# Performance work log

Hardware: AMD Instinct MI355X
Metric: run time of the kernel (lower is better)

## Reference

```python
import jax, jax.numpy as jnp
import numpy as np
import math

HIDDEN = 768
HEADS = 12
HEAD_DIM = HIDDEN // HEADS  # 64
SEQ = 197
K_RANK = min(128, HEAD_DIM)  # 64
BATCH = 64


def setup_inputs() -> dict:
    key = jax.random.key(0)
    ks = jax.random.split(key, 12)
    init = 0.02
    # Linear weights stored [in, out] (equivalent to torch W.T)
    return {
        "hidden_states": jax.random.normal(ks[0], (BATCH, SEQ, HIDDEN), dtype=jnp.float32),
        "Wq": jax.random.normal(ks[1], (HIDDEN, HIDDEN), dtype=jnp.float32) * init,
        "bq": jnp.zeros((HIDDEN,), dtype=jnp.float32),
        "Wk": jax.random.normal(ks[2], (HIDDEN, HIDDEN), dtype=jnp.float32) * init,
        "bk": jnp.zeros((HIDDEN,), dtype=jnp.float32),
        "Wv": jax.random.normal(ks[3], (HIDDEN, HIDDEN), dtype=jnp.float32) * init,
        "bv": jnp.zeros((HIDDEN,), dtype=jnp.float32),
        "Wo": jax.random.normal(ks[4], (HIDDEN, HIDDEN), dtype=jnp.float32) * init,
        "bo": jnp.zeros((HIDDEN,), dtype=jnp.float32),
        "E_k": jax.random.normal(ks[5], (SEQ, K_RANK), dtype=jnp.float32) * init,
        "E_v": jax.random.normal(ks[6], (SEQ, K_RANK), dtype=jnp.float32) * init,
    }


def reference(hidden_states, Wq, bq, Wk, bk, Wv, bv, Wo, bo, E_k, E_v):
    B, S, D = hidden_states.shape
    H, d = HEADS, HEAD_DIM
    scale = 1.0 / math.sqrt(d)

    def split_heads(x):  # [B,S,D] -> [B,H,S,d]
        return x.reshape(B, S, H, d).transpose(0, 2, 1, 3)

    q = split_heads(hidden_states @ Wq + bq)
    k = split_heads(hidden_states @ Wk + bk)
    v = split_heads(hidden_states @ Wv + bv)

    # low-rank projection of K/V along the sequence axis: [B,H,k,d]
    pk = jnp.einsum('sk,bhsd->bhkd', E_k, k)
    pv = jnp.einsum('sk,bhsd->bhkd', E_v, v)

    # scores over reduced axis: [B,H,S,k]
    scores = jnp.einsum('bhsd,bhkd->bhsk', q, pk) * scale
    probs = jax.nn.softmax(scores, axis=-1)

    ctx = jnp.einsum('bhsk,bhkd->bhsd', probs, pv)
    ctx = ctx.transpose(0, 2, 1, 3).reshape(B, S, D)
    out = ctx @ Wo + bo  # dropout rate 0.0 -> identity
    return out
```

## Files before the change

### kernel.cpp

```cpp
#include <hip/hip_runtime.h>
#include <math.h>

#define B_   64
#define S_   197
#define D_   768
#define H_   12
#define HD_  64
#define M_   (B_ * S_)
#define MPAD 12672
#define KE   224
#define BH_  (B_ * H_)
#define WSZ  ((size_t)D_ * D_)

typedef _Float16 half8_t __attribute__((ext_vector_type(8)));
typedef _Float16 half4_t __attribute__((ext_vector_type(4)));
typedef _Float16 half2_t __attribute__((ext_vector_type(2)));
typedef float floatx4 __attribute__((ext_vector_type(4)));

#define LDS_DMA16(gptr, lptr) \
  __builtin_amdgcn_global_load_lds((const __attribute__((address_space(1))) void*)(gptr), \
                                   (__attribute__((address_space(3))) void*)(lptr), 16, 0, 0)

__global__ __launch_bounds__(256) void prep_kernel(
    const float* __restrict__ X,
    const float* __restrict__ Wq, const float* __restrict__ Wk,
    const float* __restrict__ Wv, const float* __restrict__ Wo,
    const float* __restrict__ Ek, const float* __restrict__ Ev,
    _Float16* __restrict__ Xh,
    _Float16* __restrict__ Tcat, _Float16* __restrict__ To,
    _Float16* __restrict__ EET,
    float* __restrict__ esumK, float* __restrict__ esumV)
{
    __shared__ float tile[32][33];
    const int bid = blockIdx.x, tid = threadIdx.x;
    if (bid < 9504) {
        const int i4 = (bid * 256 + tid) * 4;
        float4 v = make_float4(0.f, 0.f, 0.f, 0.f);
        if (i4 < M_ * D_) v = *(const float4*)&X[i4];
        half4_t o = { (_Float16)v.x, (_Float16)v.y, (_Float16)v.z, (_Float16)v.w };
        *(half4_t*)&Xh[i4] = o;
        return;
    }
    int b2 = bid - 9504;
    if (b2 < 2304) {
        const int z = b2 / 576, rem = b2 % 576;
        const int bx = rem % 24, by = rem / 24;
        const float* W = (z == 0) ? Wk : (z == 1) ? Wv : (z == 2) ? Wq : Wo;
        _Float16* T = (z < 3) ? (Tcat + (size_t)z * WSZ) : To;
        const int n0 = bx * 32, k0 = by * 32;
        const int r = tid >> 3, c4 = (tid & 7) * 4;
        *(float4*)&tile[r][c4] = *(const float4*)&W[(size_t)(k0 + r) * D_ + n0 + c4];
        __syncthreads();
        half4_t o = { (_Float16)tile[c4 + 0][r], (_Float16)tile[c4 + 1][r],
                      (_Float16)tile[c4 + 2][r], (_Float16)tile[c4 + 3][r] };
        *(half4_t*)&T[(size_t)(n0 + r) * D_ + k0 + c4] = o;
        return;
    }
    b2 -= 2304;
    const float* E = b2 ? Ev : Ek;
    _Float16* ET = EET + (size_t)b2 * 64 * KE;
    float* es = b2 ? esumV : esumK;
    for (int i = tid; i < 64 * KE; i += 256) {
        const int rr = i / KE, s = i % KE;
        ET[i] = (_Float16)((s < S_) ? E[s * 64 + rr] : 0.f);
    }
    if (tid < 64) {
        float acc = 0.f;
        for (int s = 0; s < S_; ++s) acc += E[s * 64 + tid];
        es[tid] = acc;
    }
}

__global__ __launch_bounds__(256) void y_kernel(
    const _Float16* __restrict__ Xh, const _Float16* __restrict__ EET,
    _Float16* __restrict__ Ybuf)
{
    __shared__ _Float16 Xs[KE * 66];
    const int bid = blockIdx.x;
    const int b = bid / 12, n0 = (bid % 12) * 64;
    const int tid = threadIdx.x, w = tid >> 6, lane = tid & 63;
    const int l15 = lane & 15, quad = lane >> 4;

    #pragma unroll
    for (int i = 0; i < 7; ++i) {
        const int s = i * 32 + (tid >> 3);
        const int d0 = (tid & 7) * 8;
        const half8_t v = *(const half8_t*)&Xh[(size_t)(b * S_ + s) * D_ + n0 + d0];
        #pragma unroll
        for (int jj = 0; jj < 4; ++jj) {
            half2_t t2 = { v[2 * jj], v[2 * jj + 1] };
            *(half2_t*)&Xs[s * 66 + d0 + 2 * jj] = t2;
        }
    }
    __syncthreads();

    floatx4 acc[2][4] = {};
    #pragma unroll
    for (int k7 = 0; k7 < 7; ++k7) {
        half8_t af[2];
        #pragma unroll
        for (int mi = 0; mi < 2; ++mi)
            af[mi] = *(const half8_t*)&EET[(w * 32 + mi * 16 + l15) * KE + k7 * 32 + quad * 8];
        #pragma unroll
        for (int ni = 0; ni < 4; ++ni) {
            const int sb = k7 * 32 + quad * 8;
            half8_t bf;
            #pragma unroll
            for (int jj = 0; jj < 8; ++jj) bf[jj] = Xs[(sb + jj) * 66 + ni * 16 + l15];
            #pragma unroll
            for (int mi = 0; mi < 2; ++mi)
                acc[mi][ni] = __builtin_amdgcn_mfma_f32_16x16x32_f16(
                    af[mi], bf, acc[mi][ni], 0, 0, 0);
        }
    }

    #pragma unroll
    for (int mi = 0; mi < 2; ++mi)
        #pragma unroll
        for (int ni = 0; ni < 4; ++ni)
            #pragma unroll
            for (int i = 0; i < 4; ++i) {
                const int m_local = w * 32 + mi * 16 + quad * 4 + i;
                const int row = (m_local >> 6) * 4096 + b * 64 + (m_local & 63);
                Ybuf[(size_t)row * D_ + n0 + ni * 16 + l15] = (_Float16)acc[mi][ni][i];
            }
}

template<int MODE>
__global__ __launch_bounds__(256) void gemm_t(
    const _Float16* __restrict__ A,
    const _Float16* __restrict__ W0, const _Float16* __restrict__ W1,
    const float* __restrict__ b0, const float* __restrict__ b1,
    const float* __restrict__ es0, const float* __restrict__ es1,
    _Float16* __restrict__ O16a, _Float16* __restrict__ pvT,
    float* __restrict__ O32)
{
    __shared__ _Float16 sm[8704];
    const int xcd = blockIdx.x & 7, t = blockIdx.x >> 3;
    const int slot = t / 6, j = t - slot * 6;
    const int m_blk = slot * 8 + xcd;
    if (MODE != 1 && m_blk >= MPAD / 128) return;
    const int m0 = m_blk * 128, n0 = j * 128;
    const bool vhalf = (MODE == 1) && (m_blk >= 32);
    const _Float16* W = vhalf ? W1 : W0;
    const float* bias = vhalf ? b1 : b0;
    const float* esum = vhalf ? es1 : es0;

    const int tid = threadIdx.x;
    const int w = tid >> 6, lane = tid & 63;
    const int fr = lane & 15, quad = lane >> 4;
    const int jrow = lane >> 2;
    const int csw = ((lane & 3) ^ ((lane >> 3) & 3)) * 8;
    const int ksw = (quad ^ ((fr >> 1) & 3)) * 8;
    const int wm = (w >> 1) * 64, wn = (w & 1) * 64;

    floatx4 acc[4][4] = {};

    for (int k0 = 0; k0 < D_; k0 += 32) {
        #pragma unroll
        for (int jj = 0; jj < 2; ++jj) {
            const int r = w * 32 + jj * 16 + jrow;
            LDS_DMA16(&A[(size_t)(m0 + r) * D_ + k0 + csw],
                      &sm[w * 1024 + jj * 512]);
            LDS_DMA16(&W[(size_t)(n0 + r) * D_ + k0 + csw],
                      &sm[4096 + w * 1024 + jj * 512]);
        }
        __syncthreads();
        half8_t af[4], bf[4];
        #pragma unroll
        for (int i = 0; i < 4; ++i) {
            af[i] = *(const half8_t*)&sm[(wm + i * 16 + fr) * 32 + ksw];
            bf[i] = *(const half8_t*)&sm[4096 + (wn + i * 16 + fr) * 32 + ksw];
        }
        #pragma unroll
        for (int mi = 0; mi < 4; ++mi)
            #pragma unroll
            for (int ni = 0; ni < 4; ++ni)
                acc[mi][ni] = __builtin_amdgcn_mfma_f32_16x16x32_f16(
                    af[mi], bf[ni], acc[mi][ni], 0, 0, 0);
        __syncthreads();
    }

    float bval[4];
    #pragma unroll
    for (int ni = 0; ni < 4; ++ni)
        bval[ni] = bias[n0 + wn + ni * 16 + fr];

    if (MODE == 2) {
        const int rq = quad * 4;
        if (m0 + 128 <= M_) {
            #pragma unroll
            for (int ni = 0; ni < 4; ++ni) {
                const int n = n0 + wn + ni * 16 + fr;
                #pragma unroll
                for (int mi = 0; mi < 4; ++mi)
                    #pragma unroll
                    for (int i = 0; i < 4; ++i)
                        O32[(size_t)(m0 + wm + mi * 16 + rq + i) * D_ + n] =
                            acc[mi][ni][i] + bval[ni];
            }
        } else {
            #pragma unroll
            for (int ni = 0; ni < 4; ++ni) {
                const int n = n0 + wn + ni * 16 + fr;
                #pragma unroll
                for (int mi = 0; mi < 4; ++mi)
                    #pragma unroll
                    for (int i = 0; i < 4; ++i) {
                        const int m = m0 + wm + mi * 16 + rq + i;
                        if (m < M_)
                            O32[(size_t)m * D_ + n] = acc[mi][ni][i] + bval[ni];
                    }
            }
        }
    } else if (MODE == 1 && vhalf) {
        const int bb = (m0 - 4096 + wm) >> 6;
        #pragma unroll
        for (int mi = 0; mi < 4; ++mi) {
            const float4 es4 = *(const float4*)&esum[mi * 16 + quad * 4];
            const float esv[4] = {es4.x, es4.y, es4.z, es4.w};
            #pragma unroll
            for (int ni = 0; ni < 4; ++ni) {
                const int n = n0 + wn + ni * 16 + fr;
                const int h = n >> 6, d = n & 63;
                #pragma unroll
                for (int i = 0; i < 4; ++i) {
                    const int r = mi * 16 + quad * 4 + i;
                    pvT[((size_t)(bb * H_ + h)) * 4096 + d * 64 + r] =
                        (_Float16)(acc[mi][ni][i] + esv[i] * bval[ni]);
                }
            }
        }
    } else {
        _Float16* ct = &sm[w * 2176];
        #pragma unroll
        for (int half = 0; half < 2; ++half) {
            #pragma unroll
            for (int mi2 = 0; mi2 < 2; ++mi2) {
                const int mi = half * 2 + mi2;
                float esv[4] = {1.f, 1.f, 1.f, 1.f};
                if (MODE == 1) {
                    const float4 es4 = *(const float4*)&esum[mi * 16 + quad * 4];
                    esv[0] = es4.x; esv[1] = es4.y; esv[2] = es4.z; esv[3] = es4.w;
                }
                #pragma unroll
                for (int ni = 0; ni < 4; ++ni)
                    #pragma unroll
                    for (int i = 0; i < 4; ++i)
                        ct[(mi2 * 16 + quad * 4 + i) * 68 + ni * 16 + fr] =
                            (_Float16)(acc[mi][ni][i] + esv[i] * bval[ni]);
            }
            #pragma unroll
            for (int pass = 0; pass < 4; ++pass) {
                const int rr = pass * 8 + (lane >> 3);
                const int cc = (lane & 7) * 8;
                const half8_t v = *(const half8_t*)&ct[rr * 68 + cc];
                *(half8_t*)&O16a[(size_t)(m0 + wm + half * 32 + rr) * D_ + n0 + wn + cc] = v;
            }
        }
    }
}

__global__ __launch_bounds__(256) void attn_kernel(
    const _Float16* __restrict__ Qh, const _Float16* __restrict__ pk16,
    const _Float16* __restrict__ pvT, _Float16* __restrict__ CTXh)
{
    __shared__ _Float16 P[64 * 80];
    const int bh = blockIdx.x, b = bh / H_, h = bh % H_;
    const int tid = threadIdx.x, w = tid >> 6, lane = tid & 63;
    const int l15 = lane & 15, quad = lane >> 4;
    const _Float16* pkB = pk16 + (size_t)(b * 64) * D_ + h * 64;
    const _Float16* pvB = pvT + (size_t)bh * 4096;
    const size_t qbase = (size_t)(b * S_) * D_ + h * HD_;

    half8_t bkf[4][2], bvf[4][2];
    #pragma unroll
    for (int ni = 0; ni < 4; ++ni)
        #pragma unroll
        for (int kk = 0; kk < 2; ++kk) {
            bkf[ni][kk] = *(const half8_t*)&pkB[(size_t)(ni * 16 + l15) * D_ + kk * 32 + quad * 8];
            bvf[ni][kk] = *(const half8_t*)&pvB[(ni * 16 + l15) * 64 + kk * 32 + quad * 8];
        }

    for (int t = w; t < 13; t += 4) {
        const int srow = t * 16;
        floatx4 acc[4] = {};
        #pragma unroll
        for (int kk = 0; kk < 2; ++kk) {
            const half8_t aq = *(const half8_t*)
                &Qh[qbase + (size_t)(srow + l15) * D_ + kk * 32 + quad * 8];
            #pragma unroll
            for (int ni = 0; ni < 4; ++ni)
                acc[ni] = __builtin_amdgcn_mfma_f32_16x16x32_f16(
                    aq, bkf[ni][kk], acc[ni], 0, 0, 0);
        }
        float p[4][4];
        #pragma unroll
        for (int i = 0; i < 4; ++i) {
            const float s0 = acc[0][i] * 0.125f, s1 = acc[1][i] * 0.125f;
            const float s2 = acc[2][i] * 0.125f, s3 = acc[3][i] * 0.125f;
            float mx = fmaxf(fmaxf(s0, s1), fmaxf(s2, s3));
            #pragma unroll
            for (int off = 1; off < 16; off <<= 1)
                mx = fmaxf(mx, __shfl_xor(mx, off, 64));
            const float e0 = __expf(s0 - mx), e1 = __expf(s1 - mx);
            const float e2 = __expf(s2 - mx), e3 = __expf(s3 - mx);
            float sme = e0 + e1 + e2 + e3;
            #pragma unroll
            for (int off = 1; off < 16; off <<= 1)
                sme += __shfl_xor(sme, off, 64);
            const float inv = 1.f / sme;
            p[0][i] = e0 * inv; p[1][i] = e1 * inv;
            p[2][i] = e2 * inv; p[3][i] = e3 * inv;
        }
        #pragma unroll
        for (int ni = 0; ni < 4; ++ni)
            #pragma unroll
            for (int i = 0; i < 4; ++i)
                P[(w * 16 + quad * 4 + i) * 80 + ni * 16 + l15] = (_Float16)p[ni][i];

        floatx4 accv[4] = {};
        #pragma unroll
        for (int kk = 0; kk < 2; ++kk) {
            const half8_t ap = *(const half8_t*)&P[(w * 16 + l15) * 80 + kk * 32 + quad * 8];
            #pragma unroll
            for (int ni = 0; ni < 4; ++ni)
                accv[ni] = __builtin_amdgcn_mfma_f32_16x16x32_f16(
                    ap, bvf[ni][kk], accv[ni], 0, 0, 0);
        }
        #pragma unroll
        for (int ni = 0; ni < 4; ++ni)
            #pragma unroll
            for (int i = 0; i < 4; ++i) {
                const int s = srow + quad * 4 + i;
                if (s < S_)
                    CTXh[qbase + (size_t)s * D_ + ni * 16 + l15] = (_Float16)accv[ni][i];
            }
    }
}

extern "C" void kernel_launch(void* const* d_in, const int* in_sizes, int n_in,
                              void* d_out, int out_size, void* d_ws, size_t ws_size,
                              hipStream_t stream) {
    const float* X   = (const float*)d_in[0];
    const float* Wq  = (const float*)d_in[1];
    const float* bq  = (const float*)d_in[2];
    const float* Wk  = (const float*)d_in[3];
    const float* bk  = (const float*)d_in[4];
    const float* Wv  = (const float*)d_in[5];
    const float* bv  = (const float*)d_in[6];
    const float* Wo  = (const float*)d_in[7];
    const float* bo  = (const float*)d_in[8];
    const float* E_k = (const float*)d_in[9];
    const float* E_v = (const float*)d_in[10];
    float* out = (float*)d_out;

    char* p = (char*)d_ws;
    _Float16* Xh   = (_Float16*)p; p += (size_t)MPAD * D_ * 2;
    _Float16* Tcat = (_Float16*)p; p += (size_t)3 * WSZ * 2;
    _Float16* To   = (_Float16*)p; p += (size_t)WSZ * 2;
    _Float16* Qh   = (_Float16*)p; p += (size_t)MPAD * D_ * 2;
    _Float16* EET  = (_Float16*)p; p += (size_t)128 * KE * 2;
    float* esumK   = (float*)p;    p += 64 * sizeof(float);
    float* esumV   = (float*)p;    p += 64 * sizeof(float);
    _Float16* Ybuf = (_Float16*)p; p += (size_t)8192 * D_ * 2;
    _Float16* pk16 = (_Float16*)p; p += (size_t)4096 * D_ * 2;
    _Float16* pvT  = (_Float16*)p;

    prep_kernel<<<11810, 256, 0, stream>>>(X, Wq, Wk, Wv, Wo, E_k, E_v,
                                           Xh, Tcat, To, EET, esumK, esumV);
    y_kernel<<<768, 256, 0, stream>>>(Xh, EET, Ybuf);
    gemm_t<1><<<384, 256, 0, stream>>>(Ybuf, Tcat, Tcat + WSZ,
                                       bk, bv, esumK, esumV,
                                       pk16, pvT, nullptr);
    gemm_t<0><<<624, 256, 0, stream>>>(Xh, Tcat + 2 * WSZ, nullptr,
                                       bq, nullptr, nullptr, nullptr,
                                       Qh, nullptr, nullptr);
    attn_kernel<<<BH_, 256, 0, stream>>>(Qh, pk16, pvT, Xh);
    gemm_t<2><<<624, 256, 0, stream>>>(Xh, To, nullptr,
                                       bo, nullptr, nullptr, nullptr,
                                       nullptr, nullptr, out);
}
```

Before: 226.1 us.

## Merge Q and PK/PV GEMM launches and double K-step per LDS stage

Replaces the templated GEMM with two kernels. The Q projection and the K/V low-rank projections now run in a single launch of 1008 blocks, with a block-index split choosing the operands. Each main-loop iteration now stages a 64-wide K slice into a doubled LDS buffer with a new XOR swizzle, which halves the number of barrier pairs per tile. The output GEMM is given the same deeper K staging. The cost is twice the LDS per block, which may lower occupancy, and one larger launch in place of two.

New measurement: 218.9 us. -3.1%, faster.

```diff
diff --git a/kernel.cpp b/kernel.cpp
--- a/kernel.cpp
+++ b/kernel.cpp
@@ -126,58 +126,78 @@
             }
 }
 
-template<int MODE>
-__global__ __launch_bounds__(256) void gemm_t(
-    const _Float16* __restrict__ A,
-    const _Float16* __restrict__ W0, const _Float16* __restrict__ W1,
-    const float* __restrict__ b0, const float* __restrict__ b1,
-    const float* __restrict__ es0, const float* __restrict__ es1,
-    _Float16* __restrict__ O16a, _Float16* __restrict__ pvT,
-    float* __restrict__ O32)
+
+__global__ __launch_bounds__(256) void gemm_qpkv(
+    const _Float16* __restrict__ Xh, const _Float16* __restrict__ Ybuf,
+    const _Float16* __restrict__ Tcat,
+    const float* __restrict__ bq, const float* __restrict__ bk,
+    const float* __restrict__ bv,
+    const float* __restrict__ esumK, const float* __restrict__ esumV,
+    _Float16* __restrict__ Qh, _Float16* __restrict__ pk16,
+    _Float16* __restrict__ pvT)
 {
-    __shared__ _Float16 sm[8704];
-    const int xcd = blockIdx.x & 7, t = blockIdx.x >> 3;
-    const int slot = t / 6, j = t - slot * 6;
-    const int m_blk = slot * 8 + xcd;
-    if (MODE != 1 && m_blk >= MPAD / 128) return;
-    const int m0 = m_blk * 128, n0 = j * 128;
-    const bool vhalf = (MODE == 1) && (m_blk >= 32);
-    const _Float16* W = vhalf ? W1 : W0;
-    const float* bias = vhalf ? b1 : b0;
-    const float* esum = vhalf ? es1 : es0;
+    __shared__ _Float16 sm[16384];
+    const int bid = blockIdx.x;
+    const _Float16 *A, *W;
+    const float *bias, *esum;
+    _Float16* O16;
+    bool pvmode = false;
+    int m0, n0;
+    if (bid < 624) {
+        const int xcd = bid & 7, t = bid >> 3;
+        const int slot = t / 6, j = t - slot * 6;
+        const int m_blk = slot * 8 + xcd;
+        if (m_blk >= MPAD / 128) return;
+        m0 = m_blk * 128; n0 = j * 128;
+        A = Xh; W = Tcat + 2 * WSZ + (size_t)n0 * D_;
+        bias = bq; esum = nullptr; O16 = Qh;
+    } else {
+        const int b2 = bid - 624;
+        const int xcd = b2 & 7, t = b2 >> 3;
+        const int slot = t / 6, j = t - slot * 6;
+        const int m_blk = slot * 8 + xcd;
+        m0 = m_blk * 128; n0 = j * 128;
+        pvmode = (m_blk >= 32);
+        A = Ybuf; W = Tcat + (pvmode ? WSZ : 0) + (size_t)n0 * D_;
+        bias = pvmode ? bv : bk; esum = pvmode ? esumV : esumK;
+        O16 = pk16;
+    }
 
     const int tid = threadIdx.x;
     const int w = tid >> 6, lane = tid & 63;
-    const int fr = lane & 15, quad = lane >> 4;
-    const int jrow = lane >> 2;
-    const int csw = ((lane & 3) ^ ((lane >> 3) & 3)) * 8;
-    const int ksw = (quad ^ ((fr >> 1) & 3)) * 8;
+    const int fr = lane & 15, quad = lane >> 4, f7 = lane & 7;
+    const int l3 = lane >> 3;
+    const int csrc = ((lane & 7) ^ l3) * 8;
     const int wm = (w >> 1) * 64, wn = (w & 1) * 64;
 
+    const _Float16* Abase = A + (size_t)(m0 + w * 32 + l3) * D_ + csrc;
+    const _Float16* Wbase = W + (size_t)(w * 32 + l3) * D_ + csrc;
+
     floatx4 acc[4][4] = {};
 
-    for (int k0 = 0; k0 < D_; k0 += 32) {
-        #pragma unroll
-        for (int jj = 0; jj < 2; ++jj) {
-            const int r = w * 32 + jj * 16 + jrow;
-            LDS_DMA16(&A[(size_t)(m0 + r) * D_ + k0 + csw],
-                      &sm[w * 1024 + jj * 512]);
-            LDS_DMA16(&W[(size_t)(n0 + r) * D_ + k0 + csw],
-                      &sm[4096 + w * 1024 + jj * 512]);
+    for (int k0 = 0; k0 < D_; k0 += 64) {
+        #pragma unroll
+        for (int j = 0; j < 4; ++j) {
+            LDS_DMA16(Abase + (size_t)(j * 8) * D_ + k0, &sm[w * 2048 + j * 512]);
+            LDS_DMA16(Wbase + (size_t)(j * 8) * D_ + k0, &sm[8192 + w * 2048 + j * 512]);
         }
         __syncthreads();
-        half8_t af[4], bf[4];
-        #pragma unroll
-        for (int i = 0; i < 4; ++i) {
-            af[i] = *(const half8_t*)&sm[(wm + i * 16 + fr) * 32 + ksw];
-            bf[i] = *(const half8_t*)&sm[4096 + (wn + i * 16 + fr) * 32 + ksw];
-        }
-        #pragma unroll
-        for (int mi = 0; mi < 4; ++mi)
-            #pragma unroll
-            for (int ni = 0; ni < 4; ++ni)
-                acc[mi][ni] = __builtin_amdgcn_mfma_f32_16x16x32_f16(
-                    af[mi], bf[ni], acc[mi][ni], 0, 0, 0);
+        #pragma unroll
+        for (int ksub = 0; ksub < 2; ++ksub) {
+            const int sa = ((ksub * 4 + quad) ^ f7) * 8;
+            half8_t af[4], bf[4];
+            #pragma unroll
+            for (int i = 0; i < 4; ++i) {
+                af[i] = *(const half8_t*)&sm[(wm + i * 16 + fr) * 64 + sa];
+                bf[i] = *(const half8_t*)&sm[8192 + (wn + i * 16 + fr) * 64 + sa];
+            }
+            #pragma unroll
+            for (int mi = 0; mi < 4; ++mi)
+                #pragma unroll
+                for (int ni = 0; ni < 4; ++ni)
+                    acc[mi][ni] = __builtin_amdgcn_mfma_f32_16x16x32_f16(
+                        af[mi], bf[ni], acc[mi][ni], 0, 0, 0);
+        }
         __syncthreads();
     }
 
@@ -186,34 +206,7 @@
     for (int ni = 0; ni < 4; ++ni)
         bval[ni] = bias[n0 + wn + ni * 16 + fr];
 
-    if (MODE == 2) {
-        const int rq = quad * 4;
-        if (m0 + 128 <= M_) {
-            #pragma unroll
-            for (int ni = 0; ni < 4; ++ni) {
-                const int n = n0 + wn + ni * 16 + fr;
-                #pragma unroll
-                for (int mi = 0; mi < 4; ++mi)
-                    #pragma unroll
-                    for (int i = 0; i < 4; ++i)
-                        O32[(size_t)(m0 + wm + mi * 16 + rq + i) * D_ + n] =
-                            acc[mi][ni][i] + bval[ni];
-            }
-        } else {
-            #pragma unroll
-            for (int ni = 0; ni < 4; ++ni) {
-                const int n = n0 + wn + ni * 16 + fr;
-                #pragma unroll
-                for (int mi = 0; mi < 4; ++mi)
-                    #pragma unroll
-                    for (int i = 0; i < 4; ++i) {
-                        const int m = m0 + wm + mi * 16 + rq + i;
-                        if (m < M_)
-                            O32[(size_t)m * D_ + n] = acc[mi][ni][i] + bval[ni];
-                    }
-            }
-        }
-    } else if (MODE == 1 && vhalf) {
+    if (pvmode) {
         const int bb = (m0 - 4096 + wm) >> 6;
         #pragma unroll
         for (int mi = 0; mi < 4; ++mi) {
@@ -239,7 +232,7 @@
             for (int mi2 = 0; mi2 < 2; ++mi2) {
                 const int mi = half * 2 + mi2;
                 float esv[4] = {1.f, 1.f, 1.f, 1.f};
-                if (MODE == 1) {
+                if (esum) {
                     const float4 es4 = *(const float4*)&esum[mi * 16 + quad * 4];
                     esv[0] = es4.x; esv[1] = es4.y; esv[2] = es4.z; esv[3] = es4.w;
                 }
@@ -255,8 +248,90 @@
                 const int rr = pass * 8 + (lane >> 3);
                 const int cc = (lane & 7) * 8;
                 const half8_t v = *(const half8_t*)&ct[rr * 68 + cc];
-                *(half8_t*)&O16a[(size_t)(m0 + wm + half * 32 + rr) * D_ + n0 + wn + cc] = v;
-            }
+                *(half8_t*)&O16[(size_t)(m0 + wm + half * 32 + rr) * D_ + n0 + wn + cc] = v;
+            }
+        }
+    }
+}
+
+__global__ __launch_bounds__(256) void gemm_o(
+    const _Float16* __restrict__ CTX, const _Float16* __restrict__ To,
+    const float* __restrict__ bo, float* __restrict__ O32)
+{
+    __shared__ _Float16 sm[16384];
+    const int xcd = blockIdx.x & 7, t = blockIdx.x >> 3;
+    const int slot = t / 6, j = t - slot * 6;
+    const int m_blk = slot * 8 + xcd;
+    if (m_blk >= MPAD / 128) return;
+    const int m0 = m_blk * 128, n0 = j * 128;
+
+    const int tid = threadIdx.x;
+    const int w = tid >> 6, lane = tid & 63;
+    const int fr = lane & 15, quad = lane >> 4, f7 = lane & 7;
+    const int l3 = lane >> 3;
+    const int csrc = ((lane & 7) ^ l3) * 8;
+    const int wm = (w >> 1) * 64, wn = (w & 1) * 64;
+
+    const _Float16* Abase = CTX + (size_t)(m0 + w * 32 + l3) * D_ + csrc;
+    const _Float16* Wbase = To + (size_t)(n0 + w * 32 + l3) * D_ + csrc;
+
+    floatx4 acc[4][4] = {};
+
+    for (int k0 = 0; k0 < D_; k0 += 64) {
+        #pragma unroll
+        for (int j2 = 0; j2 < 4; ++j2) {
+            LDS_DMA16(Abase + (size_t)(j2 * 8) * D_ + k0, &sm[w * 2048 + j2 * 512]);
+            LDS_DMA16(Wbase + (size_t)(j2 * 8) * D_ + k0, &sm[8192 + w * 2048 + j2 * 512]);
+        }
+        __syncthreads();
+        #pragma unroll
+        for (int ksub = 0; ksub < 2; ++ksub) {
+            const int sa = ((ksub * 4 + quad) ^ f7) * 8;
+            half8_t af[4], bf[4];
+            #pragma unroll
+            for (int i = 0; i < 4; ++i) {
+                af[i] = *(const half8_t*)&sm[(wm + i * 16 + fr) * 64 + sa];
+                bf[i] = *(const half8_t*)&sm[8192 + (wn + i * 16 + fr) * 64 + sa];
+            }
+            #pragma unroll
+            for (int mi = 0; mi < 4; ++mi)
+                #pragma unroll
+                for (int ni = 0; ni < 4; ++ni)
+                    acc[mi][ni] = __builtin_amdgcn_mfma_f32_16x16x32_f16(
+                        af[mi], bf[ni], acc[mi][ni], 0, 0, 0);
+        }
+        __syncthreads();
+    }
+
+    float bval[4];
+    #pragma unroll
+    for (int ni = 0; ni < 4; ++ni)
+        bval[ni] = bo[n0 + wn + ni * 16 + fr];
+
+    const int rq = quad * 4;
+    if (m0 + 128 <= M_) {
+        #pragma unroll
+        for (int ni = 0; ni < 4; ++ni) {
+            const int n = n0 + wn + ni * 16 + fr;
+            #pragma unroll
+            for (int mi = 0; mi < 4; ++mi)
+                #pragma unroll
+                for (int i = 0; i < 4; ++i)
+                    O32[(size_t)(m0 + wm + mi * 16 + rq + i) * D_ + n] =
+                        acc[mi][ni][i] + bval[ni];
+        }
+    } else {
+        #pragma unroll
+        for (int ni = 0; ni < 4; ++ni) {
+            const int n = n0 + wn + ni * 16 + fr;
+            #pragma unroll
+            for (int mi = 0; mi < 4; ++mi)
+                #pragma unroll
+                for (int i = 0; i < 4; ++i) {
+                    const int m = m0 + wm + mi * 16 + rq + i;
+                    if (m < M_)
+                        O32[(size_t)m * D_ + n] = acc[mi][ni][i] + bval[ni];
+                }
         }
     }
 }
@@ -370,14 +445,9 @@
     prep_kernel<<<11810, 256, 0, stream>>>(X, Wq, Wk, Wv, Wo, E_k, E_v,
                                            Xh, Tcat, To, EET, esumK, esumV);
     y_kernel<<<768, 256, 0, stream>>>(Xh, EET, Ybuf);
-    gemm_t<1><<<384, 256, 0, stream>>>(Ybuf, Tcat, Tcat + WSZ,
-                                       bk, bv, esumK, esumV,
-                                       pk16, pvT, nullptr);
-    gemm_t<0><<<624, 256, 0, stream>>>(Xh, Tcat + 2 * WSZ, nullptr,
-                                       bq, nullptr, nullptr, nullptr,
-                                       Qh, nullptr, nullptr);
+    gemm_qpkv<<<1008, 256, 0, stream>>>(Xh, Ybuf, Tcat,
+                                        bq, bk, bv, esumK, esumV,
+                                        Qh, pk16, pvT);
     attn_kernel<<<BH_, 256, 0, stream>>>(Qh, pk16, pvT, Xh);
-    gemm_t<2><<<624, 256, 0, stream>>>(Xh, To, nullptr,
-                                       bo, nullptr, nullptr, nullptr,
-                                       nullptr, nullptr, out);
-}
+    gemm_o<<<624, 256, 0, stream>>>(Xh, To, bo, out);
+}
```
